# Optimization experiments

Measured on AMD Instinct MI355X. Metric: run time of the kernel, lower is better.

Reference implementation:

```python
import jax, jax.numpy as jnp
import numpy as np

R = 16
ALPHA = 32
SCALING = ALPHA / R  # 2.0


def setup_inputs() -> dict:
    key = jax.random.key(0)
    k_x, k_w, k_b, k_a, k_lb, k_o = jax.random.split(key, 6)
    in_f, out_f = 4096, 4096
    x = jax.random.normal(k_x, (4, 4096, in_f), dtype=jnp.float32)
    base_kernel = jax.random.normal(k_w, (in_f, out_f), dtype=jnp.float32) * 0.02
    base_bias = jax.random.normal(k_b, (out_f,), dtype=jnp.float32) * 0.02
    lora_A = jax.random.normal(k_a, (R, R), dtype=jnp.float32)
    lora_B = jax.random.normal(k_lb, (R, R), dtype=jnp.float32) * 0.02
    O = jax.random.normal(k_o, (in_f // R, out_f // R), dtype=jnp.float32)
    return {"x": x, "base_kernel": base_kernel, "base_bias": base_bias,
            "lora_A": lora_A, "lora_B": lora_B, "O": O}


def reference(x, base_kernel, base_bias, lora_A, lora_B, O) -> jnp.ndarray:
    in_f, out_f = base_kernel.shape
    # base path: x @ W + b
    base_out = jnp.dot(x, base_kernel) + base_bias
    # LoKr path: kron(A @ B, O) materialized as in the original module
    w_left = jnp.dot(lora_A, lora_B)                 # (r, r)
    lokr_update = jnp.kron(w_left, O)                # (r*in_factor, r*out_factor)
    lokr_update = lokr_update[:in_f, :out_f]
    lokr_out = jnp.dot(x, lokr_update)
    return base_out + lokr_out * SCALING
```

## Files before the change

### kernel.cpp

```cpp
#include <hip/hip_runtime.h>
#include <stdint.h>
#include <stddef.h>


#define M_TOT 16384
#define K_TOT 4096
#define N_TOT 4096
#define SCALING 2.0f

typedef __attribute__((ext_vector_type(8))) short bf16x8;
typedef __attribute__((ext_vector_type(4))) float floatx4;

__device__ __forceinline__ unsigned short f32_to_bf16(float f) {
  union { float f; unsigned int u; } v; v.f = f;
  unsigned int r = 0x7fffu + ((v.u >> 16) & 1u);
  return (unsigned short)((v.u + r) >> 16);
}

__device__ __forceinline__ void async_copy16(const void* gsrc, void* ldst) {
  __builtin_amdgcn_global_load_lds(
      (const __attribute__((address_space(1))) void*)(uintptr_t)gsrc,
      (__attribute__((address_space(3))) void*)(uintptr_t)ldst,
      16, 0, 0);
}

__global__ void wleft_kernel(const float* __restrict__ A, const float* __restrict__ B,
                             float* __restrict__ wl) {
  int i = threadIdx.x >> 4, j = threadIdx.x & 15;
  float s = 0.f;
#pragma unroll
  for (int k = 0; k < 16; ++k) s += A[i * 16 + k] * B[k * 16 + j];
  wl[threadIdx.x] = s * SCALING;
}

__global__ void prep_w_kernel(const float* __restrict__ base, const float* __restrict__ O,
                              const float* __restrict__ wl, unsigned short* __restrict__ Wt) {
  __shared__ float tile[32][33];
  int n0 = blockIdx.x * 32, k0 = blockIdx.y * 32;
  int tx = threadIdx.x, ty = threadIdx.y;
#pragma unroll
  for (int r = 0; r < 32; r += 8) {
    int k = k0 + ty + r, n = n0 + tx;
    float v = base[(size_t)k * N_TOT + n]
            + wl[((k >> 8) << 4) + (n >> 8)] * O[((size_t)(k & 255) << 8) + (n & 255)];
    tile[ty + r][tx] = v;
  }
  __syncthreads();
#pragma unroll
  for (int r = 0; r < 32; r += 8) {
    int n = n0 + ty + r, k = k0 + tx;
    Wt[(size_t)n * K_TOT + k] = f32_to_bf16(tile[tx][ty + r]);
  }
}

__global__ void cvt_x_kernel(const float* __restrict__ x, unsigned short* __restrict__ xb) {
  size_t i = ((size_t)blockIdx.x * blockDim.x + threadIdx.x) * 8;
  float4 a = *(const float4*)(x + i);
  float4 b = *(const float4*)(x + i + 4);
  union { bf16x8 v; unsigned short h[8]; } u;
  u.h[0] = f32_to_bf16(a.x); u.h[1] = f32_to_bf16(a.y);
  u.h[2] = f32_to_bf16(a.z); u.h[3] = f32_to_bf16(a.w);
  u.h[4] = f32_to_bf16(b.x); u.h[5] = f32_to_bf16(b.y);
  u.h[6] = f32_to_bf16(b.z); u.h[7] = f32_to_bf16(b.w);
  *(bf16x8*)(xb + i) = u.v;
}

__global__ __launch_bounds__(256) void gemm_bt_kernel(
    const unsigned short* __restrict__ Xb, const unsigned short* __restrict__ Wt,
    const float* __restrict__ bias, float* __restrict__ out) {
  __shared__ __align__(16) unsigned short Alds[128 * 32];
  __shared__ __align__(16) unsigned short Blds[128 * 32];

  const int tid = threadIdx.x;
  const int wave = tid >> 6, lane = tid & 63;
  const int quad = lane >> 4, lanemod = lane & 15;
  const int wm = wave & 1, wn = wave >> 1;

  const int m0 = blockIdx.y * 128, n0 = blockIdx.x * 128;

  floatx4 acc[4][4];
#pragma unroll
  for (int i = 0; i < 4; ++i)
#pragma unroll
    for (int j = 0; j < 4; ++j) acc[i][j] = (floatx4){0.f, 0.f, 0.f, 0.f};

  for (int k0 = 0; k0 < K_TOT; k0 += 32) {
#pragma unroll
    for (int it = 0; it < 2; ++it) {
      int c = it * 256 + tid;
      int row = c >> 2, kc = c & 3;
      async_copy16(Xb + ((size_t)(m0 + row) * K_TOT + k0 + kc * 8), Alds + (size_t)c * 8);
      async_copy16(Wt + ((size_t)(n0 + row) * K_TOT + k0 + kc * 8), Blds + (size_t)c * 8);
    }
    __syncthreads();

    bf16x8 af[4], bfr[4];
#pragma unroll
    for (int t = 0; t < 4; ++t) {
      af[t]  = *(const bf16x8*)(Alds + ((wm * 64 + t * 16 + lanemod) * 32 + quad * 8));
      bfr[t] = *(const bf16x8*)(Blds + ((wn * 64 + t * 16 + lanemod) * 32 + quad * 8));
    }
#pragma unroll
    for (int mt = 0; mt < 4; ++mt)
#pragma unroll
      for (int nt = 0; nt < 4; ++nt)
        acc[mt][nt] = __builtin_amdgcn_mfma_f32_16x16x32_bf16(af[mt], bfr[nt], acc[mt][nt], 0, 0, 0);
    __syncthreads();
  }

#pragma unroll
  for (int nt = 0; nt < 4; ++nt) {
    int col = n0 + wn * 64 + nt * 16 + lanemod;
    float bv = bias[col];
#pragma unroll
    for (int mt = 0; mt < 4; ++mt) {
      int row = m0 + wm * 64 + mt * 16 + quad * 4;
#pragma unroll
      for (int r = 0; r < 4; ++r)
        out[(size_t)(row + r) * N_TOT + col] = acc[mt][nt][r] + bv;
    }
  }
}

extern "C" void kernel_launch(void* const* d_in, const int* in_sizes, int n_in,
                              void* d_out, int out_size, void* d_ws, size_t ws_size,
                              hipStream_t stream) {
  const float* x    = (const float*)d_in[0];
  const float* base = (const float*)d_in[1];
  const float* bias = (const float*)d_in[2];
  const float* lA   = (const float*)d_in[3];
  const float* lB   = (const float*)d_in[4];
  const float* O    = (const float*)d_in[5];
  float* out = (float*)d_out;

  char* ws = (char*)d_ws;
  unsigned short* Xb = (unsigned short*)ws;
  unsigned short* Wt = (unsigned short*)(ws + (size_t)M_TOT * K_TOT * 2);
  float* wl = (float*)(ws + (size_t)M_TOT * K_TOT * 2 + (size_t)N_TOT * K_TOT * 2);

  wleft_kernel<<<1, 256, 0, stream>>>(lA, lB, wl);
  prep_w_kernel<<<dim3(N_TOT / 32, K_TOT / 32), dim3(32, 8), 0, stream>>>(base, O, wl, Wt);
  cvt_x_kernel<<<((size_t)M_TOT * K_TOT) / 8 / 256, 256, 0, stream>>>(x, Xb);
  gemm_bt_kernel<<<dim3(N_TOT / 128, M_TOT / 128), 256, 0, stream>>>(Xb, Wt, bias, out);
}
```

Baseline: 1.124 ms.

## Rewrite GEMM as 256x256 tile with multi-stage async LDS pipeline

Replaces the 128x128 single-buffered GEMM with a 256x256 tile over 512 threads (8 waves, 128x64 per wave). Global-to-LDS async copies are spread over four stages with partial vmcnt waits, so loads overlap the MFMA work. It also adds an XOR-swizzled LDS layout to avoid bank conflicts, a grid swizzle for L2 locality, and s_setprio around the MFMAs. In exchange it uses 128KB of LDS and more registers per thread, which may limit occupancy, and the hand-tuned waitcnt logic is fragile.

```diff
diff --git a/kernel.cpp b/kernel.cpp
--- a/kernel.cpp
+++ b/kernel.cpp
@@ -7,6 +7,7 @@
 #define K_TOT 4096
 #define N_TOT 4096
 #define SCALING 2.0f
+#define NT (K_TOT / 64)
 
 typedef __attribute__((ext_vector_type(8))) short bf16x8;
 typedef __attribute__((ext_vector_type(4))) float floatx4;
@@ -65,59 +66,103 @@
   *(bf16x8*)(xb + i) = u.v;
 }
 
-__global__ __launch_bounds__(256) void gemm_bt_kernel(
+__global__ __launch_bounds__(512, 2) void gemm256_kernel(
     const unsigned short* __restrict__ Xb, const unsigned short* __restrict__ Wt,
     const float* __restrict__ bias, float* __restrict__ out) {
-  __shared__ __align__(16) unsigned short Alds[128 * 32];
-  __shared__ __align__(16) unsigned short Blds[128 * 32];
+  __shared__ __align__(16) unsigned short lds[65536];
 
   const int tid = threadIdx.x;
   const int wave = tid >> 6, lane = tid & 63;
-  const int quad = lane >> 4, lanemod = lane & 15;
-  const int wm = wave & 1, wn = wave >> 1;
+  const int quad = lane >> 4, lm = lane & 15;
+  const int wm = wave >> 2, wn = wave & 3;
 
-  const int m0 = blockIdx.y * 128, n0 = blockIdx.x * 128;
+  const int wg = blockIdx.x;
+  const int swz = (wg & 7) * (1024 / 8) + (wg >> 3);
+  const int m0 = (swz >> 4) * 256;
+  const int n0 = (swz & 15) * 256;
 
-  floatx4 acc[4][4];
+  const int sch = (tid & 7) ^ ((tid >> 3) & 7);
+  const int rowoff = 2 * (tid >> 3) + (sch >> 2);
+  const int koff = (sch & 3) * 8;
+  const unsigned short* srcA = Xb + (size_t)(m0 + rowoff) * K_TOT + koff;
+  const unsigned short* srcB = Wt + (size_t)(n0 + rowoff) * K_TOT + koff;
+
+  const int pch = (((lm & 1) << 2) | quad) ^ (lm >> 1);
+  const int aoff = wm * 4096 + (lm >> 1) * 64 + pch * 8;
+  const int boff = wn * 2048 + (lm >> 1) * 64 + pch * 8;
+
+  floatx4 acc[8][4];
 #pragma unroll
-  for (int i = 0; i < 4; ++i)
+  for (int i = 0; i < 8; ++i)
 #pragma unroll
     for (int j = 0; j < 4; ++j) acc[i][j] = (floatx4){0.f, 0.f, 0.f, 0.f};
 
-  for (int k0 = 0; k0 < K_TOT; k0 += 32) {
-#pragma unroll
-    for (int it = 0; it < 2; ++it) {
-      int c = it * 256 + tid;
-      int row = c >> 2, kc = c & 3;
-      async_copy16(Xb + ((size_t)(m0 + row) * K_TOT + k0 + kc * 8), Alds + (size_t)c * 8);
-      async_copy16(Wt + ((size_t)(n0 + row) * K_TOT + k0 + kc * 8), Blds + (size_t)c * 8);
-    }
-    __syncthreads();
+#define STAGE(tt, ss) do {                                                        \
+    unsigned short* la = lds + ((((tt) & 1) * 2 + (ss)) * 8192) + tid * 8;        \
+    size_t kk = (size_t)(tt) * 64 + (ss) * 32;                                    \
+    async_copy16(srcA + kk, la);                                                  \
+    async_copy16(srcA + kk + (size_t)128 * K_TOT, la + 4096);                     \
+    async_copy16(srcB + kk, la + 32768);                                          \
+    async_copy16(srcB + kk + (size_t)128 * K_TOT, la + 32768 + 4096);             \
+  } while (0)
 
-    bf16x8 af[4], bfr[4];
-#pragma unroll
-    for (int t = 0; t < 4; ++t) {
-      af[t]  = *(const bf16x8*)(Alds + ((wm * 64 + t * 16 + lanemod) * 32 + quad * 8));
-      bfr[t] = *(const bf16x8*)(Blds + ((wn * 64 + t * 16 + lanemod) * 32 + quad * 8));
-    }
-#pragma unroll
-    for (int mt = 0; mt < 4; ++mt)
-#pragma unroll
-      for (int nt = 0; nt < 4; ++nt)
-        acc[mt][nt] = __builtin_amdgcn_mfma_f32_16x16x32_bf16(af[mt], bfr[nt], acc[mt][nt], 0, 0, 0);
-    __syncthreads();
+#define COMPUTE(tt, ss) do {                                                      \
+    const unsigned short* Ab = lds + ((((tt) & 1) * 2 + (ss)) * 8192) + aoff;     \
+    const unsigned short* Bb = lds + 32768 + ((((tt) & 1) * 2 + (ss)) * 8192) + boff; \
+    bf16x8 af[8], bfr[4];                                                         \
+    _Pragma("unroll") for (int i = 0; i < 8; ++i)                                 \
+      af[i] = *(const bf16x8*)(Ab + i * 512);                                     \
+    _Pragma("unroll") for (int j = 0; j < 4; ++j)                                 \
+      bfr[j] = *(const bf16x8*)(Bb + j * 512);                                    \
+    __builtin_amdgcn_s_setprio(1);                                                \
+    _Pragma("unroll") for (int i = 0; i < 8; ++i)                                 \
+      _Pragma("unroll") for (int j = 0; j < 4; ++j)                               \
+        acc[i][j] = __builtin_amdgcn_mfma_f32_16x16x32_bf16(af[i], bfr[j], acc[i][j], 0, 0, 0); \
+    __builtin_amdgcn_s_setprio(0);                                                \
+  } while (0)
+
+#define WAITBAR(n) do {                                                          \
+    asm volatile("s_waitcnt vmcnt(" #n ")" ::: "memory");                        \
+    __builtin_amdgcn_s_barrier();                                                \
+    asm volatile("" ::: "memory");                                               \
+  } while (0)
+
+  STAGE(0, 0);
+  STAGE(0, 1);
+  STAGE(1, 0);
+  WAITBAR(8);
+
+  for (int t = 0; t < NT - 2; ++t) {
+    STAGE(t + 1, 1);
+    COMPUTE(t, 0);
+    WAITBAR(8);
+    STAGE(t + 2, 0);
+    COMPUTE(t, 1);
+    WAITBAR(8);
   }
+  STAGE(NT - 1, 1);
+  COMPUTE(NT - 2, 0);
+  WAITBAR(8);
+  COMPUTE(NT - 2, 1);
+  WAITBAR(4);
+  COMPUTE(NT - 1, 0);
+  WAITBAR(0);
+  COMPUTE(NT - 1, 1);
+
+#undef STAGE
+#undef COMPUTE
+#undef WAITBAR
 
 #pragma unroll
-  for (int nt = 0; nt < 4; ++nt) {
-    int col = n0 + wn * 64 + nt * 16 + lanemod;
+  for (int j = 0; j < 4; ++j) {
+    int col = n0 + wn * 64 + j * 16 + lm;
     float bv = bias[col];
 #pragma unroll
-    for (int mt = 0; mt < 4; ++mt) {
-      int row = m0 + wm * 64 + mt * 16 + quad * 4;
+    for (int i = 0; i < 8; ++i) {
+      int row = m0 + wm * 128 + i * 16 + quad * 4;
 #pragma unroll
       for (int r = 0; r < 4; ++r)
-        out[(size_t)(row + r) * N_TOT + col] = acc[mt][nt][r] + bv;
+        out[(size_t)(row + r) * N_TOT + col] = acc[i][j][r] + bv;
     }
   }
 }
@@ -141,5 +186,5 @@
   wleft_kernel<<<1, 256, 0, stream>>>(lA, lB, wl);
   prep_w_kernel<<<dim3(N_TOT / 32, K_TOT / 32), dim3(32, 8), 0, stream>>>(base, O, wl, Wt);
   cvt_x_kernel<<<((size_t)M_TOT * K_TOT) / 8 / 256, 256, 0, stream>>>(x, Xb);
-  gemm_bt_kernel<<<dim3(N_TOT / 128, M_TOT / 128), 256, 0, stream>>>(Xb, Wt, bias, out);
+  gemm256_kernel<<<dim3(1024), 512, 0, stream>>>(Xb, Wt, bias, out);
 }
```

Result: faster. 959.1 us (-14.7%).
